# Performance work log

Measured on AMD Instinct MI355X. Metric: run time of the kernel, lower is better.

The kernel has to match this reference:

```python
import math
import jax, jax.numpy as jnp
import numpy as np

N = 2048
HID = 1024
ALPHA = 0.5
BETA = 0.1  # greedy term is zero when coords is None


def setup_inputs() -> dict:
    key = jax.random.key(0)
    k1, k2, k3, k4 = jax.random.split(key, 4)
    node_emb = jax.random.normal(k1, (N, HID), jnp.float32)
    demands = jax.random.uniform(k2, (N,), jnp.float32)  # each < 1 << capacity
    # query_net: Linear(hid+2 -> hid); key_net: Linear(hid -> hid)
    Wq = jax.random.normal(k3, (HID, HID + 2), jnp.float32) / math.sqrt(HID + 2)
    bq = jnp.zeros((HID,), jnp.float32)
    Wk = jax.random.normal(k4, (HID, HID), jnp.float32) / math.sqrt(HID)
    bk = jnp.zeros((HID,), jnp.float32)
    return {"node_emb": node_emb, "demands": demands, "Wq": Wq, "bq": bq,
            "Wk": Wk, "bk": bk, "capacity": 40, "depot_idx": 0}


def _decode(node_emb, demands, Wq, bq, Wk, bk, capacity, depot_idx):
    n, h = node_emb.shape
    cap = jnp.float32(capacity)
    inv_sqrt = 1.0 / math.sqrt(h)
    # key_net is a per-node linear map: precompute once (same math as per-step gather+linear)
    K = node_emb @ Wk.T + bk  # [N, H]
    idx = jnp.arange(n)
    # demands < 1, capacity = 40 => >= 39 customers per route => few depot returns;
    # T = N + N//8 safely bounds customer picks + route-closing depot emissions.
    T = n + n // 8
    visited0 = jnp.zeros((n,), bool).at[depot_idx].set(True)

    def step(carry, _):
        visited, load, last, done = carry
        feasible = (~visited) & (demands <= load)
        has_cand = jnp.any(feasible)
        # context = [emb(last), load/capacity, avgd]; avgd = 0 since coords is None
        ctx = jnp.concatenate([node_emb[last],
                               jnp.stack([load / cap, jnp.float32(0.0)])])
        q = Wq @ ctx + bq                      # [H]
        s = ALPHA * ((K @ q) * inv_sqrt)       # [N] scores over all nodes
        s_m = jnp.where(feasible, s, -jnp.inf)
        cand = jnp.argmax(s_m)
        take = has_cand & (~done)
        nxt = jnp.where(take, cand, depot_idx).astype(jnp.int32)
        step_score = jnp.where(take, s[cand], jnp.float32(0.0))
        visited = visited | ((idx == cand) & take)
        load = jnp.where(take, load - demands[cand], cap)  # route end resets load
        done = done | ((~take) & jnp.all(visited))
        return (visited, load, nxt, done), (nxt, step_score)

    carry0 = (visited0, cap, jnp.int32(depot_idx), jnp.bool_(False))
    _, (seq, scores) = jax.lax.scan(step, carry0, None, length=T)
    tour = jnp.concatenate([jnp.array([depot_idx], seq.dtype), seq])  # [T+1]
    return tour, scores


def reference(node_emb, demands, Wq, bq, Wk, bk, capacity, depot_idx):
    # tour: flat visitation order; routes are the segments between depot occurrences
    # (trailing depots are padding once all customers are served).
    # scores: selected decoder score at each step (0 at depot/padding steps).
    return _decode(node_emb, demands, Wq, bq, Wk, bk, capacity, depot_idx)
```

## Files before the change

kernel.cpp:

```cpp
#include <hip/hip_runtime.h>
#include <hip/hip_bf16.h>


#define NN 2048
#define HH 1024
#define TSTEPS (NN + NN / 8)
#define TILE 64
#define KT 16
#define KCAND 128
#define KL 15

__global__ __launch_bounds__(256) void prep_wqh(const float* __restrict__ Wq,
                                                float* __restrict__ Wqh) {
  int id = blockIdx.x * 256 + threadIdx.x;
  int r = id >> 10, c = id & 1023;
  Wqh[id] = Wq[r * (HH + 2) + c];
}

__global__ __launch_bounds__(256) void gemm_nt(const float* __restrict__ A, int lda,
                                               const float* __restrict__ B, int ldb,
                                               float* __restrict__ C, int ldc,
                                               int K, const float* __restrict__ bias) {
  __shared__ float As[KT][TILE + 4];
  __shared__ float Bs[KT][TILE + 4];
  const int i0 = blockIdx.y * TILE;
  const int j0 = blockIdx.x * TILE;
  const int t = threadIdx.x;
  const int srow = t >> 2, sq = t & 3;
  const int tx = t & 15, ty = t >> 4;
  float acc[4][4] = {};
  for (int k0 = 0; k0 < K; k0 += KT) {
    float4 av = *(const float4*)&A[(size_t)(i0 + srow) * lda + k0 + sq * 4];
    float4 bv = *(const float4*)&B[(size_t)(j0 + srow) * ldb + k0 + sq * 4];
    __syncthreads();
    As[sq * 4 + 0][srow] = av.x; As[sq * 4 + 1][srow] = av.y;
    As[sq * 4 + 2][srow] = av.z; As[sq * 4 + 3][srow] = av.w;
    Bs[sq * 4 + 0][srow] = bv.x; Bs[sq * 4 + 1][srow] = bv.y;
    Bs[sq * 4 + 2][srow] = bv.z; Bs[sq * 4 + 3][srow] = bv.w;
    __syncthreads();
#pragma unroll
    for (int k = 0; k < KT; ++k) {
      float4 a4 = *(const float4*)&As[k][ty * 4];
      float4 b4 = *(const float4*)&Bs[k][tx * 4];
      float a[4] = {a4.x, a4.y, a4.z, a4.w};
      float b[4] = {b4.x, b4.y, b4.z, b4.w};
#pragma unroll
      for (int m = 0; m < 4; ++m)
#pragma unroll
        for (int n = 0; n < 4; ++n) acc[m][n] = fmaf(a[m], b[n], acc[m][n]);
    }
  }
  float bb[4] = {0.f, 0.f, 0.f, 0.f};
  if (bias) {
#pragma unroll
    for (int n = 0; n < 4; ++n) bb[n] = bias[j0 + tx * 4 + n];
  }
#pragma unroll
  for (int m = 0; m < 4; ++m) {
    float4 st = {acc[m][0] + bb[0], acc[m][1] + bb[1], acc[m][2] + bb[2], acc[m][3] + bb[3]};
    *(float4*)&C[(size_t)(i0 + ty * 4 + m) * ldc + j0 + tx * 4] = st;
  }
}

__global__ __launch_bounds__(64) void uv_k(const float* __restrict__ Kmat,
                                           const float* __restrict__ Wq,
                                           const float* __restrict__ bq,
                                           float* __restrict__ u, float* __restrict__ v) {
  int i = blockIdx.x;
  int lane = threadIdx.x;
  float su = 0.f, sv = 0.f;
#pragma unroll
  for (int m = 0; m < HH / 64; ++m) {
    int j = lane + 64 * m;
    float kv = Kmat[(size_t)i * HH + j];
    su = fmaf(kv, Wq[(size_t)j * (HH + 2) + HH], su);
    sv = fmaf(kv, bq[j], sv);
  }
#pragma unroll
  for (int off = 32; off; off >>= 1) {
    su += __shfl_down(su, off, 64);
    sv += __shfl_down(sv, off, 64);
  }
  if (lane == 0) { u[i] = su; v[i] = sv; }
}

__global__ __launch_bounds__(256) void umax_k(const float* __restrict__ u,
                                              float* __restrict__ umaxp) {
  __shared__ float sm[256];
  int t = threadIdx.x;
  float m = 0.f;
  for (int i = t; i < NN; i += 256) m = fmaxf(m, fabsf(u[i]));
  sm[t] = m;
  __syncthreads();
  for (int s = 128; s; s >>= 1) {
    if (t < s) sm[t] = fmaxf(sm[t], sm[t + s]);
    __syncthreads();
  }
  if (t == 0) *umaxp = sm[0];
}

__device__ __forceinline__ unsigned f2key(float f) {
  unsigned x = __float_as_uint(f);
  return x ^ ((x >> 31) ? 0xFFFFFFFFu : 0x80000000u);
}
__device__ __forceinline__ float key2f(unsigned k) {
  unsigned x = (k & 0x80000000u) ? (k ^ 0x80000000u) : ~k;
  return __uint_as_float(x);
}
__global__ __launch_bounds__(256) void prep_cand(const float* __restrict__ GT,
                                                 uint2* __restrict__ cand,
                                                 float* __restrict__ thr,
                                                 unsigned* __restrict__ pc16,
                                                 float* __restrict__ thr16) {
  __shared__ float rowv[NN];
  __shared__ int hist[256];
  __shared__ unsigned c128k[KCAND];
  __shared__ int c128i[KCAND];
  __shared__ int s_d, s_need, s_gt, s_eq, s_gt2, s_eq2, s_flag;
  const int row = blockIdx.x, t = threadIdx.x;
  for (int i = t; i < NN; i += 256) rowv[i] = GT[(size_t)row * NN + i];
  __syncthreads();
  unsigned prefix = 0;
  int need = KCAND;
  for (int pass = 0; pass < 4; ++pass) {
    hist[t] = 0;
    __syncthreads();
    const int shift = 24 - 8 * pass;
    for (int i = t; i < NN; i += 256) {
      unsigned k = f2key(rowv[i]);
      if (pass == 0 || (k >> (shift + 8)) == (prefix >> (shift + 8)))
        atomicAdd(&hist[(k >> shift) & 0xFF], 1);
    }
    __syncthreads();
    if (t == 0) {
      int cum = 0, d = 255;
      for (; d > 0; --d) {
        if (cum + hist[d] >= need) break;
        cum += hist[d];
      }
      s_d = d;
      s_need = need - cum;
    }
    __syncthreads();
    prefix |= ((unsigned)s_d) << shift;
    need = s_need;
    __syncthreads();
  }
  const unsigned thrk = prefix;
  if (t == 0) { s_gt = 0; s_eq = 0; thr[row] = key2f(thrk); }
  __syncthreads();
  for (int i = t; i < NN; i += 256) {
    unsigned k = f2key(rowv[i]);
    if (k > thrk) {
      int p = atomicAdd(&s_gt, 1);
      cand[(size_t)row * KCAND + p] = make_uint2(__float_as_uint(rowv[i]), (unsigned)i);
      c128k[p] = k;
      c128i[p] = i;
    }
  }
  __syncthreads();
  const int cgt = s_gt;
  for (int i = t; i < NN; i += 256) {
    if (f2key(rowv[i]) == thrk) {
      int p = atomicAdd(&s_eq, 1);
      if (p < KCAND - cgt) {
        cand[(size_t)row * KCAND + cgt + p] = make_uint2(__float_as_uint(rowv[i]), (unsigned)i);
        c128k[cgt + p] = thrk;
        c128i[cgt + p] = i;
      }
    }
  }
  __syncthreads();
  unsigned pfx2 = 0;
  need = KL;
  for (int pass = 0; pass < 4; ++pass) {
    hist[t] = 0;
    __syncthreads();
    const int shift = 24 - 8 * pass;
    for (int i = t; i < KCAND; i += 256) {
      unsigned k = c128k[i];
      if (pass == 0 || (k >> (shift + 8)) == (pfx2 >> (shift + 8)))
        atomicAdd(&hist[(k >> shift) & 0xFF], 1);
    }
    __syncthreads();
    if (t == 0) {
      int cum = 0, d = 255;
      for (; d > 0; --d) {
        if (cum + hist[d] >= need) break;
        cum += hist[d];
      }
      s_d = d;
      s_need = need - cum;
    }
    __syncthreads();
    pfx2 |= ((unsigned)s_d) << shift;
    need = s_need;
    __syncthreads();
  }
  const unsigned thrk15 = pfx2;
  if (t == 0) { s_gt2 = 0; s_eq2 = 0; s_flag = 0; }
  __syncthreads();
  for (int i = t; i < KCAND; i += 256) {
    if (c128k[i] > thrk15) {
      int p = atomicAdd(&s_gt2, 1);
      pc16[(size_t)row * KL + p] = (c128k[i] & 0xFFFFF800u) | (unsigned)c128i[i];
      if (fabsf(key2f(c128k[i])) >= 128.0f) s_flag = 1;
    }
  }
  __syncthreads();
  const int cgt2 = s_gt2;
  for (int i = t; i < KCAND; i += 256) {
    if (c128k[i] == thrk15) {
      int p = atomicAdd(&s_eq2, 1);
      if (p < KL - cgt2)
        pc16[(size_t)row * KL + cgt2 + p] = (thrk15 & 0xFFFFF800u) | (unsigned)c128i[i];
    }
  }
  if (t == 0 && fabsf(key2f(thrk15)) >= 128.0f) s_flag = 1;
  __syncthreads();
  if (t == 0) thr16[row] = s_flag ? __builtin_inff() : key2f(thrk15);
}

__global__ __launch_bounds__(256) void warm_k(const float* __restrict__ a, int n,
                                              const float* __restrict__ b, int m,
                                              float* __restrict__ sink) {
  float s = 0.f;
  const float4* a4 = (const float4*)a;
  for (int i = threadIdx.x; i < n / 4; i += 256) {
    float4 x = a4[i];
    s += x.x + x.y + x.z + x.w;
  }
  for (int i = threadIdx.x; i < m; i += 256) s += b[i];
  if (s == 1.2345e-30f) sink[blockIdx.x] = s;
}

#define DPP_MERGE2(CTRL)                                                      \
  {                                                                           \
    int ovb = __builtin_amdgcn_update_dpp(                                    \
        (int)0xFF800000, __float_as_int(bv), (CTRL), 0xf, 0xf, false);        \
    int oib = __builtin_amdgcn_update_dpp(                                    \
        0x7fffffff, bi, (CTRL), 0xf, 0xf, false);                             \
    float ov = __int_as_float(ovb);                                           \
    if (ov > bv || (ov == bv && oib < bi)) { bv = ov; bi = oib; }             \
  }

#define DPP_TOP2(CTRL)                                                        \
  {                                                                           \
    int ovb = __builtin_amdgcn_update_dpp(                                    \
        (int)0xFF800000, __float_as_int(bv1), (CTRL), 0xf, 0xf, false);       \
    int oib = __builtin_amdgcn_update_dpp(                                    \
        0x7fffffff, bi1, (CTRL), 0xf, 0xf, false);                            \
    int ov2b = __builtin_amdgcn_update_dpp(                                   \
        (int)0xFF800000, __float_as_int(bv2), (CTRL), 0xf, 0xf, false);       \
    float ov1 = __int_as_float(ovb);                                          \
    float ov2 = __int_as_float(ov2b);                                         \
    float lose = fminf(bv1, ov1);                                             \
    if (ov1 > bv1 || (ov1 == bv1 && oib < bi1)) { bv1 = ov1; bi1 = oib; }     \
    bv2 = fmaxf(fmaxf(bv2, ov2), lose);                                       \
  }

__global__ __launch_bounds__(64, 1) void decode(const float* __restrict__ GT,
                                                const uint2* __restrict__ cand,
                                                const float* __restrict__ thrp,
                                                const unsigned* __restrict__ pc16,
                                                const float* __restrict__ thr16,
                                                const float* __restrict__ umaxp,
                                                const float* __restrict__ u,
                                                const float* __restrict__ demands,
                                                const int* __restrict__ capp,
                                                const int* __restrict__ depotp,
                                                float* __restrict__ out) {
  __shared__ __align__(16) unsigned s_pc[NN * KL + 64];
  __shared__ __align__(16) float s_dd[NN];
  __shared__ __align__(16) float s_u[NN];
  __shared__ __align__(16) float s_thr[NN];
  __shared__ __align__(16) float s_lr[TSTEPS];
  __shared__ __align__(16) unsigned short s_tour[TSTEPS + 2];

  const int lane = threadIdx.x;
  const int depot = *depotp;
  const float capf = (float)(*capp);
  const float umaxv = *umaxp;
  const float INF = __builtin_inff();
  const float NEGINF = -INF;
  const float C0 = 0.015625f;
  const float MARGIN = 0.5f;
  const float EGM = 0.0625f;

  for (int i = lane; i < NN; i += 64) {
    s_dd[i] = demands[i];
    s_u[i] = u[i];
    s_thr[i] = thr16[i];
  }
  {
    const uint4* p4 = (const uint4*)pc16;
    uint4* q4 = (uint4*)s_pc;
    for (int i = lane; i < NN * KL / 4; i += 64) q4[i] = p4[i];
  }
  if (lane == 0) {
    s_dd[depot] = INF;
    s_tour[0] = (unsigned short)depot;
  }

  int done = 0, ntaken = 0, lasts = depot;
  float load = capf;
  float lr = load / capf;
  int step = 0;
  uint4 cc0, cc1, cc2;
  float th0, th1, th2;

#define STEP_ONE(CC, TH)                                                        \
  {                                                                             \
    if (done) goto FLUSH;                                                       \
    const int row = lasts;                                                      \
                          \
    CC = ((const uint4*)(cand + (size_t)row * KCAND))[lane];                    \
    TH = thrp[row];                                                             \
                                \
    unsigned pw = s_pc[row * KL + lane];                                        \
    float thr1 = s_thr[row];                                                    \
    int i1x = (int)(pw & 0x7FFu);                                               \
    float g1 = key2f(pw & 0xFFFFF800u);         \
    float d1 = s_dd[i1x];                                                       \
    float su1 = s_u[i1x];                                                       \
    float t1 = fmaf(su1, lr, g1);                                               \
    bool act = (lane < KL) && (d1 <= load);                                     \
    float bv1 = act ? t1 : NEGINF;                                              \
    int bi1 = act ? i1x : 0x7fffffff;                                           \
    float bv2 = NEGINF;                                                         \
    DPP_TOP2(0x111); DPP_TOP2(0x112); DPP_TOP2(0x114);                          \
    DPP_TOP2(0x118); DPP_TOP2(0x142); DPP_TOP2(0x143);                          \
    float rv1 = __int_as_float(__builtin_amdgcn_readlane(__float_as_int(bv1), 63)); \
    int ri1 = __builtin_amdgcn_readlane(bi1, 63);                               \
    float rv2 = __int_as_float(__builtin_amdgcn_readlane(__float_as_int(bv2), 63)); \
    const float B1 = fmaf(lr, umaxv, thr1) + MARGIN;                            \
    int take, nxt;                                                              \
    if (rv1 > B1 && rv1 > rv2 + EGM) {                                          \
            \
      take = 1; nxt = ri1;                                                      \
    } else {                                                                    \
           \
      float bv = NEGINF;                                                        \
      int bi = 0x7fffffff;                                                      \
      {                                                                         \
        float ga = __uint_as_float(CC.x); int ia = (int)CC.y;                   \
        float gb = __uint_as_float(CC.z); int ib = (int)CC.w;                   \
        float da = s_dd[ia], ua = s_u[ia];                                      \
        float db = s_dd[ib], ub = s_u[ib];                                      \
        float ta = fmaf(ua, lr, ga);                                            \
        float tb = fmaf(ub, lr, gb);                                            \
        if ((da <= load) && (ta > bv || (ta == bv && ia < bi))) { bv = ta; bi = ia; } \
        if ((db <= load) && (tb > bv || (tb == bv && ib < bi))) { bv = tb; bi = ib; } \
      }                                                                         \
      DPP_MERGE2(0x111); DPP_MERGE2(0x112); DPP_MERGE2(0x114);                  \
      DPP_MERGE2(0x118); DPP_MERGE2(0x142); DPP_MERGE2(0x143);                  \
      float rbv = __int_as_float(__builtin_amdgcn_readlane(__float_as_int(bv), 63)); \
      int rbi = __builtin_amdgcn_readlane(bi, 63);                              \
      const float B2 = fmaf(lr, umaxv, TH) + MARGIN;                            \
      if (rbv > B2) {                                                           \
        take = 1; nxt = rbi;                                                    \
      } else {                                                                  \
                              \
        const float4* rowp = (const float4*)(GT + (size_t)row * NN);            \
        const float4* dd4 = (const float4*)s_dd;                                \
        const float4* uu4 = (const float4*)s_u;                                 \
        float fv = NEGINF;                                                      \
        int fi = NN;                                                            \
        _Pragma("unroll") for (int r = 0; r < 8; ++r) {                         \
          float4 g4 = rowp[r * 64 + lane];                                      \
          float4 d4v = dd4[r * 64 + lane];                                      \
          float4 u4v = uu4[r * 64 + lane];                                      \
          float gl[4] = {g4.x, g4.y, g4.z, g4.w};                               \
          float dl[4] = {d4v.x, d4v.y, d4v.z, d4v.w};                           \
          float ul[4] = {u4v.x, u4v.y, u4v.z, u4v.w};                           \
          float cv = NEGINF;                                                    \
          int cj = 0;                                                           \
          _Pragma("unroll") for (int j = 0; j < 4; ++j) {                       \
            float tt = fmaf(ul[j], lr, gl[j]);                                  \
            bool feas = (dl[j] <= load);                                        \
            if (feas && tt > cv) { cv = tt; cj = j; }                           \
          }                                                                     \
          if (cv > fv) { fv = cv; fi = 4 * (r * 64 + lane) + cj; }              \
        }                                                                       \
        float bv = fv;                                                          \
        int bi = fi;                                                            \
        DPP_MERGE2(0x111); DPP_MERGE2(0x112); DPP_MERGE2(0x114);                \
        DPP_MERGE2(0x118); DPP_MERGE2(0x142); DPP_MERGE2(0x143);                \
        float fbv = __int_as_float(__builtin_amdgcn_readlane(__float_as_int(bv), 63)); \
        int fbi = __builtin_amdgcn_readlane(bi, 63);                            \
        take = (fbv > NEGINF) ? 1 : 0;                                          \
        nxt = take ? fbi : depot;                                               \
      }                                                                         \
    }                                                                           \
        \
    if (lane == 0) {                                                            \
      s_tour[1 + step] = (unsigned short)nxt;                                   \
      s_lr[step] = take ? lr : -1.0f;                                           \
    }                                                                           \
    if (take) {                                                                 \
      float dwin = s_dd[nxt];          \
      load = load - dwin;                                                       \
      ntaken++;                                                                 \
      if (lane == 0) s_dd[nxt] = INF;                                           \
    } else {                                                                    \
      load = capf;                                                              \
      if (ntaken == NN - 1) done = 1;                                           \
    }                                                                           \
    lasts = nxt;                                                                \
    lr = load / capf;                                                           \
    ++step;                                                                     \
  }

  for (int s3 = 0; s3 < TSTEPS; s3 += 3) {
    STEP_ONE(cc0, th0)
    STEP_ONE(cc1, th1)
    STEP_ONE(cc2, th2)
  }
FLUSH:
  for (int q = step + lane; q < TSTEPS; q += 64) {
    s_tour[1 + q] = (unsigned short)depot;
    s_lr[q] = -1.0f;
  }
  for (int i = lane; i <= TSTEPS; i += 64) out[i] = (float)s_tour[i];
  for (int s = lane; s < TSTEPS; s += 64) {
    float lrs = s_lr[s];
    float sc = 0.0f;
    if (lrs >= 0.0f) {
      int lastI = (int)s_tour[s];
      int biI = (int)s_tour[s + 1];
      float g = GT[(size_t)lastI * NN + biI];
      sc = fmaf(s_u[biI], lrs, g) * C0;
    }
    out[1 + TSTEPS + s] = sc;
  }
#undef STEP_ONE
}

extern "C" void kernel_launch(void* const* d_in, const int* in_sizes, int n_in,
                              void* d_out, int out_size, void* d_ws, size_t ws_size,
                              hipStream_t stream) {
  const float* emb     = (const float*)d_in[0];
  const float* demands = (const float*)d_in[1];
  const float* Wq      = (const float*)d_in[2];
  const float* bq      = (const float*)d_in[3];
  const float* Wk      = (const float*)d_in[4];
  const float* bk      = (const float*)d_in[5];
  const int* cap       = (const int*)d_in[6];
  const int* depot     = (const int*)d_in[7];
  float* out           = (float*)d_out;

  char* ws = (char*)d_ws;
  float* Kmat = (float*)(ws);
  float* Z    = (float*)(ws + ((size_t)8 << 20));
  float* GT   = (float*)(ws + ((size_t)16 << 20));
  float* Wqh  = (float*)(ws + ((size_t)32 << 20));
  float* u    = (float*)(ws + ((size_t)36 << 20));
  float* v    = (float*)(ws + ((size_t)36 << 20) + 8192);
  float* thr  = (float*)(ws + ((size_t)36 << 20) + 16384);
  float* umax = (float*)(ws + ((size_t)36 << 20) + 24576);
  float* sink = (float*)(ws + ((size_t)36 << 20) + 32768);
  uint2* cnd  = (uint2*)Wqh;
  unsigned* pc16g = (unsigned*)(ws + ((size_t)34 << 20));
  float* thr16g   = (float*)(ws + ((size_t)34 << 20) + (128 << 10));

  hipLaunchKernelGGL(prep_wqh, dim3(4096), dim3(256), 0, stream, Wq, Wqh);
  hipLaunchKernelGGL(gemm_nt, dim3(HH / TILE, NN / TILE), dim3(256), 0, stream,
                     emb, HH, Wk, HH, Kmat, HH, HH, bk);
  hipLaunchKernelGGL(gemm_nt, dim3(HH / TILE, NN / TILE), dim3(256), 0, stream,
                     emb, HH, Wqh, HH, Z, HH, HH, (const float*)nullptr);
  hipLaunchKernelGGL(uv_k, dim3(NN), dim3(64), 0, stream, Kmat, Wq, bq, u, v);
  hipLaunchKernelGGL(umax_k, dim3(1), dim3(256), 0, stream, u, umax);
  hipLaunchKernelGGL(gemm_nt, dim3(NN / TILE, NN / TILE), dim3(256), 0, stream,
                     Z, HH, Kmat, HH, GT, NN, HH, v);
  hipLaunchKernelGGL(prep_cand, dim3(NN), dim3(256), 0, stream, GT, cnd, thr,
                     pc16g, thr16g);
  hipLaunchKernelGGL(warm_k, dim3(128), dim3(256), 0, stream,
                     (const float*)cnd, NN * KCAND * 2, thr, NN, sink);
  hipLaunchKernelGGL(decode, dim3(1), dim3(64), 0, stream, GT, cnd, thr,
                     pc16g, thr16g, umax, u, demands, cap, depot, out);
}
```

Before: 2.202 ms.

## Tighten decode early-exit bounds with per-row interpolated thresholds and fused demand/u layout

Prep now computes, for each row, the maximum of g+u over non-candidates and packs it with the top-15 and top-128 thresholds into bf16-rounded-up halves. Decode combines these as (1-lr)*t + lr*m, which gives a tighter bound than the old thr + lr*umax, so the cheap top-15 and top-128 paths should accept more steps and the full-row scan should run less often. Demand and u are interleaved into one float2 shared array. The winner's demand is carried through the DPP reductions, so it no longer has to be re-read after the selection. The top-15 reduction is shortened to 16 lanes, and the per-step lr is written to a global buffer instead of shared memory. The rounding-up helper has to keep the packed bounds conservative, or decode could pick the wrong node.

```diff
diff --git a/kernel.cpp b/kernel.cpp
--- a/kernel.cpp
+++ b/kernel.cpp
@@ -107,18 +107,33 @@
   unsigned x = (k & 0x80000000u) ? (k ^ 0x80000000u) : ~k;
   return __uint_as_float(x);
 }
+__device__ __forceinline__ unsigned ub16(float x) {
+  unsigned b = __float_as_uint(x);
+  if (x > 0.f && (b & 0xFFFFu)) b += 0x10000u;
+  return b >> 16;
+}
 __global__ __launch_bounds__(256) void prep_cand(const float* __restrict__ GT,
+                                                 const float* __restrict__ u,
                                                  uint2* __restrict__ cand,
-                                                 float* __restrict__ thr,
                                                  unsigned* __restrict__ pc16,
-                                                 float* __restrict__ thr16) {
+                                                 uint2* __restrict__ thrpk2) {
   __shared__ float rowv[NN];
+  __shared__ float su_[NN];
   __shared__ int hist[256];
+  __shared__ float red15[256];
+  __shared__ float red128[256];
   __shared__ unsigned c128k[KCAND];
   __shared__ int c128i[KCAND];
+  __shared__ unsigned char markA[NN];
+  __shared__ unsigned char markB[NN];
   __shared__ int s_d, s_need, s_gt, s_eq, s_gt2, s_eq2, s_flag;
   const int row = blockIdx.x, t = threadIdx.x;
-  for (int i = t; i < NN; i += 256) rowv[i] = GT[(size_t)row * NN + i];
+  for (int i = t; i < NN; i += 256) {
+    rowv[i] = GT[(size_t)row * NN + i];
+    su_[i] = u[i];
+    markA[i] = 0;
+    markB[i] = 0;
+  }
   __syncthreads();
   unsigned prefix = 0;
   int need = KCAND;
@@ -147,7 +162,7 @@
     __syncthreads();
   }
   const unsigned thrk = prefix;
-  if (t == 0) { s_gt = 0; s_eq = 0; thr[row] = key2f(thrk); }
+  if (t == 0) { s_gt = 0; s_eq = 0; }
   __syncthreads();
   for (int i = t; i < NN; i += 256) {
     unsigned k = f2key(rowv[i]);
@@ -156,6 +171,7 @@
       cand[(size_t)row * KCAND + p] = make_uint2(__float_as_uint(rowv[i]), (unsigned)i);
       c128k[p] = k;
       c128i[p] = i;
+      markA[i] = 1;
     }
   }
   __syncthreads();
@@ -167,6 +183,7 @@
         cand[(size_t)row * KCAND + cgt + p] = make_uint2(__float_as_uint(rowv[i]), (unsigned)i);
         c128k[cgt + p] = thrk;
         c128i[cgt + p] = i;
+        markA[i] = 1;
       }
     }
   }
@@ -204,6 +221,7 @@
     if (c128k[i] > thrk15) {
       int p = atomicAdd(&s_gt2, 1);
       pc16[(size_t)row * KL + p] = (c128k[i] & 0xFFFFF800u) | (unsigned)c128i[i];
+      markB[c128i[i]] = 1;
       if (fabsf(key2f(c128k[i])) >= 128.0f) s_flag = 1;
     }
   }
@@ -212,17 +230,40 @@
   for (int i = t; i < KCAND; i += 256) {
     if (c128k[i] == thrk15) {
       int p = atomicAdd(&s_eq2, 1);
-      if (p < KL - cgt2)
+      if (p < KL - cgt2) {
         pc16[(size_t)row * KL + cgt2 + p] = (thrk15 & 0xFFFFF800u) | (unsigned)c128i[i];
+        markB[c128i[i]] = 1;
+      }
     }
   }
   if (t == 0 && fabsf(key2f(thrk15)) >= 128.0f) s_flag = 1;
   __syncthreads();
-  if (t == 0) thr16[row] = s_flag ? __builtin_inff() : key2f(thrk15);
+  float lm15 = -__builtin_inff(), lm128 = -__builtin_inff();
+  for (int i = t; i < NN; i += 256) {
+    float gu = rowv[i] + su_[i];
+    if (!markB[i]) lm15 = fmaxf(lm15, gu);
+    if (!markA[i]) lm128 = fmaxf(lm128, gu);
+  }
+  red15[t] = lm15;
+  red128[t] = lm128;
+  __syncthreads();
+  for (int s = 128; s; s >>= 1) {
+    if (t < s) {
+      red15[t] = fmaxf(red15[t], red15[t + s]);
+      red128[t] = fmaxf(red128[t], red128[t + s]);
+    }
+    __syncthreads();
+  }
+  if (t == 0) {
+    const float INF = __builtin_inff();
+    float t15 = s_flag ? INF : key2f(thrk15);
+    float m15 = s_flag ? INF : red15[0];
+    thrpk2[row] = make_uint2((ub16(t15) << 16) | ub16(m15),
+                             (ub16(key2f(thrk)) << 16) | ub16(red128[0]));
+  }
 }
 
 __global__ __launch_bounds__(256) void warm_k(const float* __restrict__ a, int n,
-                                              const float* __restrict__ b, int m,
                                               float* __restrict__ sink) {
   float s = 0.f;
   const float4* a4 = (const float4*)a;
@@ -230,67 +271,70 @@
     float4 x = a4[i];
     s += x.x + x.y + x.z + x.w;
   }
-  for (int i = threadIdx.x; i < m; i += 256) s += b[i];
   if (s == 1.2345e-30f) sink[blockIdx.x] = s;
 }
 
-#define DPP_MERGE2(CTRL)                                                      \
+#define DPP_MERGE3(CTRL)                                                      \
   {                                                                           \
     int ovb = __builtin_amdgcn_update_dpp(                                    \
         (int)0xFF800000, __float_as_int(bv), (CTRL), 0xf, 0xf, false);        \
     int oib = __builtin_amdgcn_update_dpp(                                    \
         0x7fffffff, bi, (CTRL), 0xf, 0xf, false);                             \
+    int odb = __builtin_amdgcn_update_dpp(                                    \
+        0, __float_as_int(bd), (CTRL), 0xf, 0xf, false);                      \
     float ov = __int_as_float(ovb);                                           \
-    if (ov > bv || (ov == bv && oib < bi)) { bv = ov; bi = oib; }             \
-  }
-
-#define DPP_TOP2(CTRL)                                                        \
+    if (ov > bv || (ov == bv && oib < bi)) {                                  \
+      bv = ov; bi = oib; bd = __int_as_float(odb);                            \
+    }                                                                         \
+  }
+
+#define DPP_TOP2D(CTRL)                                                       \
   {                                                                           \
     int ovb = __builtin_amdgcn_update_dpp(                                    \
         (int)0xFF800000, __float_as_int(bv1), (CTRL), 0xf, 0xf, false);       \
     int oib = __builtin_amdgcn_update_dpp(                                    \
         0x7fffffff, bi1, (CTRL), 0xf, 0xf, false);                            \
+    int odb = __builtin_amdgcn_update_dpp(                                    \
+        0, __float_as_int(bd1), (CTRL), 0xf, 0xf, false);                     \
     int ov2b = __builtin_amdgcn_update_dpp(                                   \
         (int)0xFF800000, __float_as_int(bv2), (CTRL), 0xf, 0xf, false);       \
     float ov1 = __int_as_float(ovb);                                          \
     float ov2 = __int_as_float(ov2b);                                         \
     float lose = fminf(bv1, ov1);                                             \
-    if (ov1 > bv1 || (ov1 == bv1 && oib < bi1)) { bv1 = ov1; bi1 = oib; }     \
+    if (ov1 > bv1 || (ov1 == bv1 && oib < bi1)) {                             \
+      bv1 = ov1; bi1 = oib; bd1 = __int_as_float(odb);                        \
+    }                                                                         \
     bv2 = fmaxf(fmaxf(bv2, ov2), lose);                                       \
   }
 
 __global__ __launch_bounds__(64, 1) void decode(const float* __restrict__ GT,
                                                 const uint2* __restrict__ cand,
-                                                const float* __restrict__ thrp,
                                                 const unsigned* __restrict__ pc16,
-                                                const float* __restrict__ thr16,
-                                                const float* __restrict__ umaxp,
+                                                const uint2* __restrict__ thrpk2,
                                                 const float* __restrict__ u,
                                                 const float* __restrict__ demands,
                                                 const int* __restrict__ capp,
                                                 const int* __restrict__ depotp,
+                                                float* __restrict__ lrbuf,
                                                 float* __restrict__ out) {
   __shared__ __align__(16) unsigned s_pc[NN * KL + 64];
-  __shared__ __align__(16) float s_dd[NN];
-  __shared__ __align__(16) float s_u[NN];
-  __shared__ __align__(16) float s_thr[NN];
-  __shared__ __align__(16) float s_lr[TSTEPS];
+  __shared__ __align__(16) float2 s_du[NN];
+  __shared__ __align__(16) uint2 s_thr[NN];
   __shared__ __align__(16) unsigned short s_tour[TSTEPS + 2];
 
   const int lane = threadIdx.x;
   const int depot = *depotp;
   const float capf = (float)(*capp);
-  const float umaxv = *umaxp;
   const float INF = __builtin_inff();
   const float NEGINF = -INF;
   const float C0 = 0.015625f;
   const float MARGIN = 0.5f;
   const float EGM = 0.0625f;
+  float* sduf = (float*)s_du;
 
   for (int i = lane; i < NN; i += 64) {
-    s_dd[i] = demands[i];
-    s_u[i] = u[i];
-    s_thr[i] = thr16[i];
+    s_du[i] = make_float2(demands[i], u[i]);
+    s_thr[i] = thrpk2[i];
   }
   {
     const uint4* p4 = (const uint4*)pc16;
@@ -298,7 +342,7 @@
     for (int i = lane; i < NN * KL / 4; i += 64) q4[i] = p4[i];
   }
   if (lane == 0) {
-    s_dd[depot] = INF;
+    sduf[2 * depot] = INF;
     s_tour[0] = (unsigned short)depot;
   }
 
@@ -306,73 +350,84 @@
   float load = capf;
   float lr = load / capf;
   int step = 0;
+  const int lcl = (lane < KL) ? lane : (KL - 1);
   uint4 cc0, cc1, cc2;
-  float th0, th1, th2;
-
-#define STEP_ONE(CC, TH)                                                        \
+
+#define STEP_ONE(CC)                                                            \
   {                                                                             \
     if (done) goto FLUSH;                                                       \
     const int row = lasts;                                                      \
-                          \
+     \
     CC = ((const uint4*)(cand + (size_t)row * KCAND))[lane];                    \
-    TH = thrp[row];                                                             \
-                                \
-    unsigned pw = s_pc[row * KL + lane];                                        \
-    float thr1 = s_thr[row];                                                    \
+           \
+    unsigned pw = s_pc[row * KL + lcl];                                         \
+    uint2 pk2 = s_thr[row];                                                     \
     int i1x = (int)(pw & 0x7FFu);                                               \
     float g1 = key2f(pw & 0xFFFFF800u);         \
-    float d1 = s_dd[i1x];                                                       \
-    float su1 = s_u[i1x];                                                       \
-    float t1 = fmaf(su1, lr, g1);                                               \
-    bool act = (lane < KL) && (d1 <= load);                                     \
+    float2 du1 = s_du[i1x];                                \
+    float t1 = fmaf(du1.y, lr, g1);                                             \
+    bool act = (lane < KL) && (du1.x <= load);                                  \
     float bv1 = act ? t1 : NEGINF;                                              \
     int bi1 = act ? i1x : 0x7fffffff;                                           \
+    float bd1 = act ? du1.x : 0.f;                                              \
     float bv2 = NEGINF;                                                         \
-    DPP_TOP2(0x111); DPP_TOP2(0x112); DPP_TOP2(0x114);                          \
-    DPP_TOP2(0x118); DPP_TOP2(0x142); DPP_TOP2(0x143);                          \
-    float rv1 = __int_as_float(__builtin_amdgcn_readlane(__float_as_int(bv1), 63)); \
-    int ri1 = __builtin_amdgcn_readlane(bi1, 63);                               \
-    float rv2 = __int_as_float(__builtin_amdgcn_readlane(__float_as_int(bv2), 63)); \
-    const float B1 = fmaf(lr, umaxv, thr1) + MARGIN;                            \
+    DPP_TOP2D(0x111); DPP_TOP2D(0x112); DPP_TOP2D(0x114); DPP_TOP2D(0x118);     \
+    float rv1 = __int_as_float(__builtin_amdgcn_readlane(__float_as_int(bv1), 15)); \
+    int ri1 = __builtin_amdgcn_readlane(bi1, 15);                               \
+    float rv2 = __int_as_float(__builtin_amdgcn_readlane(__float_as_int(bv2), 15)); \
+    float rd1 = __int_as_float(__builtin_amdgcn_readlane(__float_as_int(bd1), 15)); \
+            \
+    float t15 = __uint_as_float(pk2.x & 0xFFFF0000u);                           \
+    float m15 = __uint_as_float(pk2.x << 16);                                   \
+    float B1 = fmaf(1.0f - lr, t15, lr * m15) + MARGIN;                         \
     int take, nxt;                                                              \
+    float dwin;                                                                 \
     if (rv1 > B1 && rv1 > rv2 + EGM) {                                          \
-            \
-      take = 1; nxt = ri1;                                                      \
+                    \
+      take = 1; nxt = ri1; dwin = rd1;                                          \
     } else {                                                                    \
-           \
+       \
       float bv = NEGINF;                                                        \
       int bi = 0x7fffffff;                                                      \
+      float bd = 0.f;                                                           \
       {                                                                         \
         float ga = __uint_as_float(CC.x); int ia = (int)CC.y;                   \
         float gb = __uint_as_float(CC.z); int ib = (int)CC.w;                   \
-        float da = s_dd[ia], ua = s_u[ia];                                      \
-        float db = s_dd[ib], ub = s_u[ib];                                      \
-        float ta = fmaf(ua, lr, ga);                                            \
-        float tb = fmaf(ub, lr, gb);                                            \
-        if ((da <= load) && (ta > bv || (ta == bv && ia < bi))) { bv = ta; bi = ia; } \
-        if ((db <= load) && (tb > bv || (tb == bv && ib < bi))) { bv = tb; bi = ib; } \
+        float2 da = s_du[ia];                                                   \
+        float2 db = s_du[ib];                                                   \
+        float ta = fmaf(da.y, lr, ga);                                          \
+        float tb = fmaf(db.y, lr, gb);                                          \
+        if ((da.x <= load) && (ta > bv || (ta == bv && ia < bi))) {             \
+          bv = ta; bi = ia; bd = da.x;                                          \
+        }                                                                       \
+        if ((db.x <= load) && (tb > bv || (tb == bv && ib < bi))) {             \
+          bv = tb; bi = ib; bd = db.x;                                          \
+        }                                                                       \
       }                                                                         \
-      DPP_MERGE2(0x111); DPP_MERGE2(0x112); DPP_MERGE2(0x114);                  \
-      DPP_MERGE2(0x118); DPP_MERGE2(0x142); DPP_MERGE2(0x143);                  \
+      DPP_MERGE3(0x111); DPP_MERGE3(0x112); DPP_MERGE3(0x114);                  \
+      DPP_MERGE3(0x118); DPP_MERGE3(0x142); DPP_MERGE3(0x143);                  \
       float rbv = __int_as_float(__builtin_amdgcn_readlane(__float_as_int(bv), 63)); \
       int rbi = __builtin_amdgcn_readlane(bi, 63);                              \
-      const float B2 = fmaf(lr, umaxv, TH) + MARGIN;                            \
+      float rbd = __int_as_float(__builtin_amdgcn_readlane(__float_as_int(bd), 63)); \
+      float t128 = __uint_as_float(pk2.y & 0xFFFF0000u);                        \
+      float m128 = __uint_as_float(pk2.y << 16);                                \
+      float B2 = fmaf(1.0f - lr, t128, lr * m128) + MARGIN;                     \
       if (rbv > B2) {                                                           \
-        take = 1; nxt = rbi;                                                    \
+        take = 1; nxt = rbi; dwin = rbd;                                        \
       } else {                                                                  \
                               \
         const float4* rowp = (const float4*)(GT + (size_t)row * NN);            \
-        const float4* dd4 = (const float4*)s_dd;                                \
-        const float4* uu4 = (const float4*)s_u;                                 \
+        const float4* du4 = (const float4*)s_du;                                \
         float fv = NEGINF;                                                      \
         int fi = NN;                                                            \
+        float fd = 0.f;                                                         \
         _Pragma("unroll") for (int r = 0; r < 8; ++r) {                         \
           float4 g4 = rowp[r * 64 + lane];                                      \
-          float4 d4v = dd4[r * 64 + lane];                                      \
-          float4 u4v = uu4[r * 64 + lane];                                      \
+          float4 pA = du4[(r * 64 + lane) * 2];                \
+          float4 pB = du4[(r * 64 + lane) * 2 + 1];            \
           float gl[4] = {g4.x, g4.y, g4.z, g4.w};                               \
-          float dl[4] = {d4v.x, d4v.y, d4v.z, d4v.w};                           \
-          float ul[4] = {u4v.x, u4v.y, u4v.z, u4v.w};                           \
+          float dl[4] = {pA.x, pA.z, pB.x, pB.z};                               \
+          float ul[4] = {pA.y, pA.w, pB.y, pB.w};                               \
           float cv = NEGINF;                                                    \
           int cj = 0;                                                           \
           _Pragma("unroll") for (int j = 0; j < 4; ++j) {                       \
@@ -380,56 +435,59 @@
             bool feas = (dl[j] <= load);                                        \
             if (feas && tt > cv) { cv = tt; cj = j; }                           \
           }                                                                     \
-          if (cv > fv) { fv = cv; fi = 4 * (r * 64 + lane) + cj; }              \
+          if (cv > fv) { fv = cv; fi = 4 * (r * 64 + lane) + cj; fd = dl[cj]; } \
         }                                                                       \
         float bv = fv;                                                          \
         int bi = fi;                                                            \
-        DPP_MERGE2(0x111); DPP_MERGE2(0x112); DPP_MERGE2(0x114);                \
-        DPP_MERGE2(0x118); DPP_MERGE2(0x142); DPP_MERGE2(0x143);                \
+        float bd = fd;                                                          \
+        DPP_MERGE3(0x111); DPP_MERGE3(0x112); DPP_MERGE3(0x114);                \
+        DPP_MERGE3(0x118); DPP_MERGE3(0x142); DPP_MERGE3(0x143);                \
         float fbv = __int_as_float(__builtin_amdgcn_readlane(__float_as_int(bv), 63)); \
         int fbi = __builtin_amdgcn_readlane(bi, 63);                            \
+        float fbd = __int_as_float(__builtin_amdgcn_readlane(__float_as_int(bd), 63)); \
         take = (fbv > NEGINF) ? 1 : 0;                                          \
         nxt = take ? fbi : depot;                                               \
+        dwin = fbd;                                                             \
       }                                                                         \
     }                                                                           \
-        \
+               \
     if (lane == 0) {                                                            \
       s_tour[1 + step] = (unsigned short)nxt;                                   \
-      s_lr[step] = take ? lr : -1.0f;                                           \
+      lrbuf[step] = take ? lr : -1.0f;        \
     }                                                                           \
     if (take) {                                                                 \
-      float dwin = s_dd[nxt];          \
-      load = load - dwin;                                                       \
+      load = load - dwin;      \
       ntaken++;                                                                 \
-      if (lane == 0) s_dd[nxt] = INF;                                           \
+      if (lane == 0) sduf[2 * nxt] = INF;                                       \
     } else {                                                                    \
       load = capf;                                                              \
       if (ntaken == NN - 1) done = 1;                                           \
     }                                                                           \
     lasts = nxt;                                                                \
-    lr = load / capf;                                                           \
+    lr = load / capf;                      \
     ++step;                                                                     \
   }
 
   for (int s3 = 0; s3 < TSTEPS; s3 += 3) {
-    STEP_ONE(cc0, th0)
-    STEP_ONE(cc1, th1)
-    STEP_ONE(cc2, th2)
+    STEP_ONE(cc0)
+    STEP_ONE(cc1)
+    STEP_ONE(cc2)
   }
 FLUSH:
   for (int q = step + lane; q < TSTEPS; q += 64) {
     s_tour[1 + q] = (unsigned short)depot;
-    s_lr[q] = -1.0f;
-  }
+    lrbuf[q] = -1.0f;
+  }
+  asm volatile("s_waitcnt vmcnt(0)" ::: "memory");
   for (int i = lane; i <= TSTEPS; i += 64) out[i] = (float)s_tour[i];
   for (int s = lane; s < TSTEPS; s += 64) {
-    float lrs = s_lr[s];
+    float lrs = lrbuf[s];
     float sc = 0.0f;
     if (lrs >= 0.0f) {
       int lastI = (int)s_tour[s];
       int biI = (int)s_tour[s + 1];
       float g = GT[(size_t)lastI * NN + biI];
-      sc = fmaf(s_u[biI], lrs, g) * C0;
+      sc = fmaf(s_du[biI].y, lrs, g) * C0;
     }
     out[1 + TSTEPS + s] = sc;
   }
@@ -456,12 +514,12 @@
   float* Wqh  = (float*)(ws + ((size_t)32 << 20));
   float* u    = (float*)(ws + ((size_t)36 << 20));
   float* v    = (float*)(ws + ((size_t)36 << 20) + 8192);
-  float* thr  = (float*)(ws + ((size_t)36 << 20) + 16384);
   float* umax = (float*)(ws + ((size_t)36 << 20) + 24576);
   float* sink = (float*)(ws + ((size_t)36 << 20) + 32768);
   uint2* cnd  = (uint2*)Wqh;
   unsigned* pc16g = (unsigned*)(ws + ((size_t)34 << 20));
-  float* thr16g   = (float*)(ws + ((size_t)34 << 20) + (128 << 10));
+  uint2* thrpk2g  = (uint2*)(ws + ((size_t)34 << 20) + (128 << 10));
+  float* lrbuf    = (float*)(ws + ((size_t)34 << 20) + (160 << 10));
 
   hipLaunchKernelGGL(prep_wqh, dim3(4096), dim3(256), 0, stream, Wq, Wqh);
   hipLaunchKernelGGL(gemm_nt, dim3(HH / TILE, NN / TILE), dim3(256), 0, stream,
@@ -472,10 +530,10 @@
   hipLaunchKernelGGL(umax_k, dim3(1), dim3(256), 0, stream, u, umax);
   hipLaunchKernelGGL(gemm_nt, dim3(NN / TILE, NN / TILE), dim3(256), 0, stream,
                      Z, HH, Kmat, HH, GT, NN, HH, v);
-  hipLaunchKernelGGL(prep_cand, dim3(NN), dim3(256), 0, stream, GT, cnd, thr,
-                     pc16g, thr16g);
+  hipLaunchKernelGGL(prep_cand, dim3(NN), dim3(256), 0, stream, GT, u, cnd,
+                     pc16g, thrpk2g);
   hipLaunchKernelGGL(warm_k, dim3(128), dim3(256), 0, stream,
-                     (const float*)cnd, NN * KCAND * 2, thr, NN, sink);
-  hipLaunchKernelGGL(decode, dim3(1), dim3(64), 0, stream, GT, cnd, thr,
-                     pc16g, thr16g, umax, u, demands, cap, depot, out);
-}
+                     (const float*)cnd, NN * KCAND * 2 + (160 << 8), sink);
+  hipLaunchKernelGGL(decode, dim3(1), dim3(64), 0, stream, GT, cnd,
+                     pc16g, thrpk2g, u, demands, cap, depot, lrbuf, out);
+}
```

Result: faster. 2.093 ms (-4.9%).
